# Kernel tuning notes

Hardware: AMD Instinct MI355X
Metric: run time of the kernel (lower is better)

The kernel has to match this reference:

```python
import jax, jax.numpy as jnp
import numpy as np

N, D = 2048, 1024
H, KV, HD = 16, 4, 64
REPEATS = H // KV
SCALE = HD ** -0.5


def setup_inputs() -> dict:
    key = jax.random.key(0)
    ks = jax.random.split(key, 6)
    x = jax.random.normal(ks[0], (N, D), dtype=jnp.float32)
    # rotary tables: cos/sin of interleaved-pair angles (llama-style view_as_complex)
    pos = jnp.arange(N, dtype=jnp.float32)[:, None]
    inv_freq = 1.0 / (10000.0 ** (jnp.arange(0, HD, 2, dtype=jnp.float32) / HD))
    ang = pos * inv_freq[None, :]  # (N, HD//2)
    freqs_cos = jnp.cos(ang)
    freqs_sin = jnp.sin(ang)
    s = 0.02
    Wq = jax.random.normal(ks[1], (D, H * HD), dtype=jnp.float32) * s
    Wk = jax.random.normal(ks[2], (D, KV * HD), dtype=jnp.float32) * s
    Wv = jax.random.normal(ks[3], (D, KV * HD), dtype=jnp.float32) * s
    Wo = jax.random.normal(ks[4], (H * HD, D), dtype=jnp.float32) * s
    return {"x": x, "freqs_cos": freqs_cos, "freqs_sin": freqs_sin,
            "Wq": Wq, "Wk": Wk, "Wv": Wv, "Wo": Wo}


def _rope(t, cos, sin):
    # t: (N, heads, HD); interleaved complex pairs (even=real, odd=imag)
    tr = t[..., 0::2]
    ti = t[..., 1::2]
    c = cos[:, None, :]
    s = sin[:, None, :]
    out_r = tr * c - ti * s
    out_i = tr * s + ti * c
    return jnp.stack([out_r, out_i], axis=-1).reshape(t.shape)


def reference(x, freqs_cos, freqs_sin, Wq, Wk, Wv, Wo):
    n = x.shape[0]
    xq = (x @ Wq).reshape(n, H, HD)
    xk = (x @ Wk).reshape(n, KV, HD)
    xv = (x @ Wv).reshape(n, KV, HD)
    xq = _rope(xq, freqs_cos, freqs_sin)
    xk = _rope(xk, freqs_cos, freqs_sin)
    # repeat_kv along head dim (GQA)
    k = jnp.repeat(xk, REPEATS, axis=1)  # (n, H, HD)
    v = jnp.repeat(xv, REPEATS, axis=1)
    # memory_efficient_attention with mask=None: full attention over token axis
    scores = jnp.einsum('nhd,mhd->hnm', xq, k) * SCALE
    attn = jax.nn.softmax(scores, axis=-1)
    out = jnp.einsum('hnm,mhd->nhd', attn, v)
    return out.reshape(n, H * HD) @ Wo
```

## Files before the change

kernel.cpp:

```cpp
#include <hip/hip_runtime.h>

#define N_TOK 2048
#define DMODEL 1024
#define NH 16
#define NKV 4
#define HDIM 64
#define SCALE_LOG2E 0.1803368801111204f

typedef __attribute__((ext_vector_type(8))) short short8;
typedef __attribute__((ext_vector_type(4))) float f32x4;
typedef unsigned short u16;
typedef unsigned int u32;

__device__ __forceinline__ u16 f2bf(float x) {
    u32 u = __float_as_uint(x);
    u += 0x7FFF + ((u >> 16) & 1);
    return (u16)(u >> 16);
}
__device__ __forceinline__ u32 pack2(float a, float b) {
    return (u32)f2bf(a) | ((u32)f2bf(b) << 16);
}
__device__ __forceinline__ u32 pack2t(float a, float b) {
    return __builtin_amdgcn_perm(__float_as_uint(b), __float_as_uint(a), 0x07060302u);
}

__global__ __launch_bounds__(256) void prep(
    const float* __restrict__ Wq, const float* __restrict__ Wk,
    const float* __restrict__ Wv, const float* __restrict__ Wo,
    const float* __restrict__ x,
    u16* __restrict__ Wqt, u16* __restrict__ Wkt, u16* __restrict__ Wvt,
    u16* __restrict__ Wot, u16* __restrict__ xb)
{
    const int z = blockIdx.z;
    const int t = threadIdx.x;
    if (z == 4) {
        size_t base = ((size_t)(blockIdx.y * 16 + blockIdx.x)) * 8192;
#pragma unroll
        for (int i = 0; i < 8; ++i) {
            float4 v = *(const float4*)(x + base + i * 1024 + t * 4);
            uint2 p; p.x = pack2(v.x, v.y); p.y = pack2(v.z, v.w);
            *(uint2*)(xb + base + i * 1024 + t * 4) = p;
        }
        return;
    }
    const float* W; u16* Wt; int NC;
    if      (z == 0) { W = Wq; Wt = Wqt; NC = 1024; }
    else if (z == 1) { W = Wk; Wt = Wkt; NC = 256; }
    else if (z == 2) { W = Wv; Wt = Wvt; NC = 256; }
    else             { W = Wo; Wt = Wot; NC = 1024; }
    const int n0 = blockIdx.x * 64;
    if (n0 >= NC) return;
    const int k0 = blockIdx.y * 64;
    __shared__ float T[64][68];
    const int row = t >> 2, cs = (t & 3) * 16;
#pragma unroll
    for (int i = 0; i < 4; ++i)
        *(float4*)&T[row][cs + i * 4] =
            *(const float4*)(W + (size_t)(k0 + row) * NC + n0 + cs + i * 4);
    __syncthreads();
    const int nl = t >> 2, ks = (t & 3) * 16;
    u32 pk[8];
#pragma unroll
    for (int i = 0; i < 8; ++i)
        pk[i] = pack2(T[ks + 2 * i][nl], T[ks + 2 * i + 1][nl]);
    u16* dst = Wt + (size_t)(n0 + nl) * DMODEL + k0 + ks;
    uint4 w0; w0.x = pk[0]; w0.y = pk[1]; w0.z = pk[2]; w0.w = pk[3];
    uint4 w1; w1.x = pk[4]; w1.y = pk[5]; w1.z = pk[6]; w1.w = pk[7];
    *(uint4*)(dst) = w0;
    *(uint4*)(dst + 8) = w1;
}

__global__ __launch_bounds__(256, 2) void gemm_qkv(
    const u16* __restrict__ A,
    const u16* __restrict__ B0, const u16* __restrict__ B1, const u16* __restrict__ B2,
    u16* __restrict__ D0, u16* __restrict__ D1, u16* __restrict__ FVout,
    const float* __restrict__ fc, const float* __restrict__ fs)
{
    __shared__ u16 As[128][40];
    __shared__ u16 Bs[128][40];
    const int t = threadIdx.x;
    const int m0 = blockIdx.x * 128;
    const int by = blockIdx.y;

    const u16* Bt; int nl0, ep;
    u16* dbf = nullptr; int dstride = 0; float epsc = 1.f;
    if (by < 8)       { Bt = B0; nl0 = by * 128;        dbf = D0; ep = 1; dstride = 1024;
                        epsc = SCALE_LOG2E; }
    else if (by < 10) { Bt = B1; nl0 = (by - 8) * 128;  dbf = D1; ep = 1; dstride = 256; }
    else              { Bt = B2; nl0 = (by - 10) * 128; ep = 2; }

    const int w = t >> 6, lane = t & 63;
    const int quad = lane >> 4, l15 = lane & 15;
    const int wm = (w >> 1) * 64, wn = (w & 1) * 64;
    const int srow = t >> 1, sk = (t & 1) * 16;

    const u16* Ap = A + (size_t)(m0 + srow) * DMODEL + sk;
    const u16* Bp = Bt + (size_t)(nl0 + srow) * DMODEL + sk;

    f32x4 acc[4][4];
#pragma unroll
    for (int i = 0; i < 4; ++i)
#pragma unroll
        for (int j = 0; j < 4; ++j) acc[i][j] = {0.f, 0.f, 0.f, 0.f};

    uint4 ar0 = *(const uint4*)(Ap);
    uint4 ar1 = *(const uint4*)(Ap + 8);
    uint4 br0 = *(const uint4*)(Bp);
    uint4 br1 = *(const uint4*)(Bp + 8);

    for (int k0 = 0; k0 < DMODEL; k0 += 32) {
        __syncthreads();
        *(uint4*)&As[srow][sk]     = ar0;
        *(uint4*)&As[srow][sk + 8] = ar1;
        *(uint4*)&Bs[srow][sk]     = br0;
        *(uint4*)&Bs[srow][sk + 8] = br1;
        __syncthreads();
        if (k0 + 32 < DMODEL) {
            ar0 = *(const uint4*)(Ap + k0 + 32);
            ar1 = *(const uint4*)(Ap + k0 + 40);
            br0 = *(const uint4*)(Bp + k0 + 32);
            br1 = *(const uint4*)(Bp + k0 + 40);
        }
        short8 af[4], bf[4];
#pragma unroll
        for (int i = 0; i < 4; ++i)
            af[i] = *(const short8*)&As[wm + i * 16 + l15][quad * 8];
#pragma unroll
        for (int j = 0; j < 4; ++j)
            bf[j] = *(const short8*)&Bs[wn + j * 16 + l15][quad * 8];
#pragma unroll
        for (int i = 0; i < 4; ++i)
#pragma unroll
            for (int j = 0; j < 4; ++j)
                acc[i][j] = __builtin_amdgcn_mfma_f32_16x16x32_bf16(af[i], bf[j], acc[i][j], 0, 0, 0);
    }

#pragma unroll
    for (int i = 0; i < 4; ++i)
#pragma unroll
        for (int j = 0; j < 4; ++j) {
            const int cl = nl0 + wn + j * 16 + l15;
#pragma unroll
            for (int r4 = 0; r4 < 4; ++r4) {
                const int r = m0 + wm + i * 16 + quad * 4 + r4;
                float own = acc[i][j][r4];
                if (ep == 1) {
                    float other = __shfl_xor(own, 1, 64);
                    const int p = (cl & 63) >> 1;
                    const float c = fc[r * 32 + p] * epsc, s = fs[r * 32 + p] * epsc;
                    float outv = ((cl & 1) == 0) ? (own * c - other * s)
                                                 : (other * s + own * c);
                    dbf[(size_t)r * dstride + cl] = f2bf(outv);
                } else {
                    const int g = cl >> 6, d = cl & 63;
                    const int dt = d >> 4, l15v = d & 15;
                    const int kt = r >> 6, klo = r & 63;
                    const int c = klo >> 5, k5 = klo & 31;
                    const int qd = k5 >> 3, jv = k5 & 7;
                    size_t idx = ((((size_t)(g * 32 + kt) * 4 + dt) * 2 + c) * 64
                                  + qd * 16 + l15v) * 8 + jv;
                    FVout[idx] = f2bf(own);
                }
            }
        }
}

__global__ __launch_bounds__(256, 2) void gemm_out(
    const u16* __restrict__ A, const u16* __restrict__ Bt, float* __restrict__ Dout)
{
    __shared__ u16 As[64][40];
    __shared__ u16 Bs[128][40];
    const int t = threadIdx.x;
    const int m0 = blockIdx.x * 64;
    const int nl0 = blockIdx.y * 128;

    const int w = t >> 6, lane = t & 63;
    const int quad = lane >> 4, l15 = lane & 15;
    const int wm = (w >> 1) * 32, wn = (w & 1) * 64;
    const int arow = t >> 2, acol = (t & 3) * 8;
    const int brow = t >> 1, bcol = (t & 1) * 16;

    const u16* Ap = A + (size_t)(m0 + arow) * DMODEL + acol;
    const u16* Bp = Bt + (size_t)(nl0 + brow) * DMODEL + bcol;

    f32x4 acc[2][4];
#pragma unroll
    for (int i = 0; i < 2; ++i)
#pragma unroll
        for (int j = 0; j < 4; ++j) acc[i][j] = {0.f, 0.f, 0.f, 0.f};

    uint4 ar  = *(const uint4*)(Ap);
    uint4 br0 = *(const uint4*)(Bp);
    uint4 br1 = *(const uint4*)(Bp + 8);

    for (int k0 = 0; k0 < DMODEL; k0 += 32) {
        __syncthreads();
        *(uint4*)&As[arow][acol]     = ar;
        *(uint4*)&Bs[brow][bcol]     = br0;
        *(uint4*)&Bs[brow][bcol + 8] = br1;
        __syncthreads();
        if (k0 + 32 < DMODEL) {
            ar  = *(const uint4*)(Ap + k0 + 32);
            br0 = *(const uint4*)(Bp + k0 + 32);
            br1 = *(const uint4*)(Bp + k0 + 40);
        }
        short8 af[2], bf[4];
#pragma unroll
        for (int i = 0; i < 2; ++i)
            af[i] = *(const short8*)&As[wm + i * 16 + l15][quad * 8];
#pragma unroll
        for (int j = 0; j < 4; ++j)
            bf[j] = *(const short8*)&Bs[wn + j * 16 + l15][quad * 8];
#pragma unroll
        for (int i = 0; i < 2; ++i)
#pragma unroll
            for (int j = 0; j < 4; ++j)
                acc[i][j] = __builtin_amdgcn_mfma_f32_16x16x32_bf16(af[i], bf[j], acc[i][j], 0, 0, 0);
    }

#pragma unroll
    for (int i = 0; i < 2; ++i)
#pragma unroll
        for (int j = 0; j < 4; ++j) {
            const int cl = nl0 + wn + j * 16 + l15;
#pragma unroll
            for (int r4 = 0; r4 < 4; ++r4) {
                const int r = m0 + wm + i * 16 + quad * 4 + r4;
                Dout[(size_t)r * 1024 + cl] = acc[i][j][r4];
            }
        }
}

__global__ __launch_bounds__(256, 2) void attn(
    const u16* __restrict__ Qb, const u16* __restrict__ Kb,
    const u16* __restrict__ FV, u16* __restrict__ Ob)
{
    __shared__ u16 Ks[2][128][72];
    __shared__ u16 Ps[4][2][16][68];

    const int t = threadIdx.x;
    const int n0 = blockIdx.x * 64;
    const int h = blockIdx.y, kvh = h >> 2;
    const int w = t >> 6, lane = t & 63;
    const int quad = lane >> 4, l15 = lane & 15;
    const int srow = t >> 1, ssel = (t & 1) * 32;

    const u16* qp = Qb + (size_t)(n0 + w * 16 + l15) * (NH * HDIM) + h * HDIM + quad * 8;
    const short8 aq0 = *(const short8*)qp;
    const short8 aq1 = *(const short8*)(qp + 32);

    const u16* kbase = Kb + (size_t)srow * (NKV * HDIM) + kvh * HDIM + ssel;
    const u16* fvb = FV + ((size_t)kvh * 32 * 4096) + (size_t)lane * 8;

    f32x4 o[4];
#pragma unroll
    for (int i = 0; i < 4; ++i) o[i] = {0.f, 0.f, 0.f, 0.f};
    float l_acc = 0.f;

#pragma unroll
    for (int c = 0; c < 4; ++c)
        *(uint4*)&Ks[0][srow][ssel + c * 8] = *(const uint4*)(kbase + c * 8);
    __syncthreads();

    for (int rd = 0; rd < 16; ++rd) {
        const int cur = rd & 1, nxt = cur ^ 1;
        const int rdn = (rd + 1) & 15;
        uint4 kr[4];
#pragma unroll
        for (int c = 0; c < 4; ++c)
            kr[c] = *(const uint4*)(kbase + (size_t)(rdn * 128) * (NKV * HDIM) + c * 8);

#pragma unroll
        for (int sub = 0; sub < 2; ++sub) {
            const int kt = rd * 2 + sub;
            short8 vf0[4], vf1[4];
#pragma unroll
            for (int dt = 0; dt < 4; ++dt) {
                vf0[dt] = *(const short8*)(fvb + (size_t)kt * 4096 + (dt * 2 + 0) * 512);
                vf1[dt] = *(const short8*)(fvb + (size_t)kt * 4096 + (dt * 2 + 1) * 512);
            }
            f32x4 s[4];
#pragma unroll
            for (int nt = 0; nt < 4; ++nt) {
                short8 kb0 = *(const short8*)&Ks[cur][sub * 64 + nt * 16 + l15][quad * 8];
                short8 kb1 = *(const short8*)&Ks[cur][sub * 64 + nt * 16 + l15][quad * 8 + 32];
                f32x4 z = {0.f, 0.f, 0.f, 0.f};
                z = __builtin_amdgcn_mfma_f32_16x16x32_bf16(kb0, aq0, z, 0, 0, 0);
                z = __builtin_amdgcn_mfma_f32_16x16x32_bf16(kb1, aq1, z, 0, 0, 0);
                s[nt] = z;
            }
#pragma unroll
            for (int nt = 0; nt < 4; ++nt) {
                float p0 = __builtin_amdgcn_exp2f(s[nt][0]);
                float p1 = __builtin_amdgcn_exp2f(s[nt][1]);
                float p2 = __builtin_amdgcn_exp2f(s[nt][2]);
                float p3 = __builtin_amdgcn_exp2f(s[nt][3]);
                l_acc += (p0 + p1) + (p2 + p3);
                uint2 pk; pk.x = pack2t(p0, p1); pk.y = pack2t(p2, p3);
                *(uint2*)&Ps[w][sub][l15][nt * 16 + quad * 4] = pk;
            }
            const short8 ap0 = *(const short8*)&Ps[w][sub][l15][quad * 8];
            const short8 ap1 = *(const short8*)&Ps[w][sub][l15][quad * 8 + 32];
#pragma unroll
            for (int dt = 0; dt < 4; ++dt) {
                o[dt] = __builtin_amdgcn_mfma_f32_16x16x32_bf16(ap0, vf0[dt], o[dt], 0, 0, 0);
                o[dt] = __builtin_amdgcn_mfma_f32_16x16x32_bf16(ap1, vf1[dt], o[dt], 0, 0, 0);
            }
        }
#pragma unroll
        for (int c = 0; c < 4; ++c)
            *(uint4*)&Ks[nxt][srow][ssel + c * 8] = kr[c];
        __syncthreads();
    }

    l_acc += __shfl_xor(l_acc, 16, 64);
    l_acc += __shfl_xor(l_acc, 32, 64);
    float linv[4];
#pragma unroll
    for (int r = 0; r < 4; ++r)
        linv[r] = 1.f / __shfl(l_acc, quad * 4 + r, 16);
#pragma unroll
    for (int dt = 0; dt < 4; ++dt)
#pragma unroll
        for (int r = 0; r < 4; ++r) {
            const int qrow = n0 + w * 16 + quad * 4 + r;
            const int col = h * HDIM + dt * 16 + l15;
            Ob[(size_t)qrow * (NH * HDIM) + col] = f2bf(o[dt][r] * linv[r]);
        }
}

extern "C" void kernel_launch(void* const* d_in, const int* in_sizes, int n_in,
                              void* d_out, int out_size, void* d_ws, size_t ws_size,
                              hipStream_t stream) {
    const float* x  = (const float*)d_in[0];
    const float* fc = (const float*)d_in[1];
    const float* fs = (const float*)d_in[2];
    const float* Wq = (const float*)d_in[3];
    const float* Wk = (const float*)d_in[4];
    const float* Wv = (const float*)d_in[5];
    const float* Wo = (const float*)d_in[6];
    float* out = (float*)d_out;

    u16* ws  = (u16*)d_ws;
    u16* xb  = ws;
    u16* Wqt = xb  + (size_t)2048 * 1024;
    u16* Wkt = Wqt + (size_t)1024 * 1024;
    u16* Wvt = Wkt + (size_t)256 * 1024;
    u16* Wot = Wvt + (size_t)256 * 1024;
    u16* qb  = Wot + (size_t)1024 * 1024;
    u16* kb  = qb  + (size_t)2048 * 1024;
    u16* fv  = kb  + (size_t)2048 * 256;
    u16* aob = fv  + (size_t)256 * 2048;

    prep<<<dim3(16, 16, 5), dim3(256), 0, stream>>>(Wq, Wk, Wv, Wo, x,
                                                    Wqt, Wkt, Wvt, Wot, xb);
    gemm_qkv<<<dim3(16, 12), dim3(256), 0, stream>>>(xb, Wqt, Wkt, Wvt,
                                                     qb, kb, fv, fc, fs);
    attn<<<dim3(32, 16), dim3(256), 0, stream>>>(qb, kb, fv, aob);
    gemm_out<<<dim3(32, 8), dim3(256), 0, stream>>>(aob, Wot, out);
}
```

Measured before the change: 157.6 us.

## Fuse all four stages into one cooperative persistent kernel with grid syncs

Replaces the four separate launches (prep, QKV GEMM, attention, output GEMM) with one cooperative kernel of 512 blocks that reuses a shared-memory union and separates the stages with grid-wide syncs. The QKV GEMM tile also shrinks from 128x128 to 64x128, so 384 blocks run instead of 192. This removes launch gaps and inter-kernel drains. In exchange it adds grid-sync overhead, leaves blocks idle in the GEMM stages, and sizes every block's shared memory to the largest stage, which may limit occupancy.

```diff
diff --git a/kernel.cpp b/kernel.cpp
--- a/kernel.cpp
+++ b/kernel.cpp
@@ -1,4 +1,7 @@
 #include <hip/hip_runtime.h>
+#include <hip/hip_cooperative_groups.h>
+
+namespace cg = cooperative_groups;
 
 #define N_TOK 2048
 #define DMODEL 1024
@@ -24,309 +27,305 @@
     return __builtin_amdgcn_perm(__float_as_uint(b), __float_as_uint(a), 0x07060302u);
 }
 
-__global__ __launch_bounds__(256) void prep(
+struct SmemPrep { float T[64][68]; };
+struct SmemGemm { u16 As[128][40]; u16 Bs[128][40]; };
+struct SmemAttn { u16 Ks[2][128][72]; u16 Ps[4][2][16][68]; };
+
+__global__ __launch_bounds__(256, 2) void fused(
+    const float* __restrict__ x, const float* __restrict__ fc,
+    const float* __restrict__ fs,
     const float* __restrict__ Wq, const float* __restrict__ Wk,
     const float* __restrict__ Wv, const float* __restrict__ Wo,
-    const float* __restrict__ x,
     u16* __restrict__ Wqt, u16* __restrict__ Wkt, u16* __restrict__ Wvt,
-    u16* __restrict__ Wot, u16* __restrict__ xb)
+    u16* __restrict__ Wot, u16* __restrict__ xb,
+    u16* __restrict__ qb, u16* __restrict__ kb, u16* __restrict__ fv,
+    u16* __restrict__ aob, float* __restrict__ out)
 {
-    const int z = blockIdx.z;
+    __shared__ alignas(16) char smem[sizeof(SmemAttn)];
     const int t = threadIdx.x;
-    if (z == 4) {
-        size_t base = ((size_t)(blockIdx.y * 16 + blockIdx.x)) * 8192;
-#pragma unroll
-        for (int i = 0; i < 8; ++i) {
-            float4 v = *(const float4*)(x + base + i * 1024 + t * 4);
-            uint2 p; p.x = pack2(v.x, v.y); p.y = pack2(v.z, v.w);
-            *(uint2*)(xb + base + i * 1024 + t * 4) = p;
+    const int bid = blockIdx.x;
+    cg::grid_group grid = cg::this_grid();
+
+    {
+        float (&T)[64][68] = reinterpret_cast<SmemPrep*>(smem)->T;
+        for (int j = bid; j < 896; j += 512) {
+            if (j >= 640) {
+                size_t base = (size_t)(j - 640) * 8192;
+#pragma unroll
+                for (int i = 0; i < 8; ++i) {
+                    float4 v = *(const float4*)(x + base + i * 1024 + t * 4);
+                    uint2 p; p.x = pack2(v.x, v.y); p.y = pack2(v.z, v.w);
+                    *(uint2*)(xb + base + i * 1024 + t * 4) = p;
+                }
+                continue;
+            }
+            const float* W; u16* Wt; int NC, xb_, yb_;
+            if (j < 256)      { W = Wq; Wt = Wqt; NC = 1024; xb_ = j & 15; yb_ = j >> 4; }
+            else if (j < 320) { W = Wk; Wt = Wkt; NC = 256;  int q = j - 256; xb_ = q & 3; yb_ = q >> 2; }
+            else if (j < 384) { W = Wv; Wt = Wvt; NC = 256;  int q = j - 320; xb_ = q & 3; yb_ = q >> 2; }
+            else              { W = Wo; Wt = Wot; NC = 1024; int q = j - 384; xb_ = q & 15; yb_ = q >> 4; }
+            const int n0 = xb_ * 64, k0 = yb_ * 64;
+            const int row = t >> 2, cs = (t & 3) * 16;
+            __syncthreads();
+#pragma unroll
+            for (int i = 0; i < 4; ++i)
+                *(float4*)&T[row][cs + i * 4] =
+                    *(const float4*)(W + (size_t)(k0 + row) * NC + n0 + cs + i * 4);
+            __syncthreads();
+            const int nl = t >> 2, ks = (t & 3) * 16;
+            u32 pk[8];
+#pragma unroll
+            for (int i = 0; i < 8; ++i)
+                pk[i] = pack2(T[ks + 2 * i][nl], T[ks + 2 * i + 1][nl]);
+            u16* dst = Wt + (size_t)(n0 + nl) * DMODEL + k0 + ks;
+            uint4 w0; w0.x = pk[0]; w0.y = pk[1]; w0.z = pk[2]; w0.w = pk[3];
+            uint4 w1; w1.x = pk[4]; w1.y = pk[5]; w1.z = pk[6]; w1.w = pk[7];
+            *(uint4*)(dst) = w0;
+            *(uint4*)(dst + 8) = w1;
         }
-        return;
     }
-    const float* W; u16* Wt; int NC;
-    if      (z == 0) { W = Wq; Wt = Wqt; NC = 1024; }
-    else if (z == 1) { W = Wk; Wt = Wkt; NC = 256; }
-    else if (z == 2) { W = Wv; Wt = Wvt; NC = 256; }
-    else             { W = Wo; Wt = Wot; NC = 1024; }
-    const int n0 = blockIdx.x * 64;
-    if (n0 >= NC) return;
-    const int k0 = blockIdx.y * 64;
-    __shared__ float T[64][68];
-    const int row = t >> 2, cs = (t & 3) * 16;
-#pragma unroll
-    for (int i = 0; i < 4; ++i)
-        *(float4*)&T[row][cs + i * 4] =
-            *(const float4*)(W + (size_t)(k0 + row) * NC + n0 + cs + i * 4);
-    __syncthreads();
-    const int nl = t >> 2, ks = (t & 3) * 16;
-    u32 pk[8];
-#pragma unroll
-    for (int i = 0; i < 8; ++i)
-        pk[i] = pack2(T[ks + 2 * i][nl], T[ks + 2 * i + 1][nl]);
-    u16* dst = Wt + (size_t)(n0 + nl) * DMODEL + k0 + ks;
-    uint4 w0; w0.x = pk[0]; w0.y = pk[1]; w0.z = pk[2]; w0.w = pk[3];
-    uint4 w1; w1.x = pk[4]; w1.y = pk[5]; w1.z = pk[6]; w1.w = pk[7];
-    *(uint4*)(dst) = w0;
-    *(uint4*)(dst + 8) = w1;
-}
-
-__global__ __launch_bounds__(256, 2) void gemm_qkv(
-    const u16* __restrict__ A,
-    const u16* __restrict__ B0, const u16* __restrict__ B1, const u16* __restrict__ B2,
-    u16* __restrict__ D0, u16* __restrict__ D1, u16* __restrict__ FVout,
-    const float* __restrict__ fc, const float* __restrict__ fs)
-{
-    __shared__ u16 As[128][40];
-    __shared__ u16 Bs[128][40];
-    const int t = threadIdx.x;
-    const int m0 = blockIdx.x * 128;
-    const int by = blockIdx.y;
-
-    const u16* Bt; int nl0, ep;
-    u16* dbf = nullptr; int dstride = 0; float epsc = 1.f;
-    if (by < 8)       { Bt = B0; nl0 = by * 128;        dbf = D0; ep = 1; dstride = 1024;
-                        epsc = SCALE_LOG2E; }
-    else if (by < 10) { Bt = B1; nl0 = (by - 8) * 128;  dbf = D1; ep = 1; dstride = 256; }
-    else              { Bt = B2; nl0 = (by - 10) * 128; ep = 2; }
-
-    const int w = t >> 6, lane = t & 63;
-    const int quad = lane >> 4, l15 = lane & 15;
-    const int wm = (w >> 1) * 64, wn = (w & 1) * 64;
-    const int srow = t >> 1, sk = (t & 1) * 16;
-
-    const u16* Ap = A + (size_t)(m0 + srow) * DMODEL + sk;
-    const u16* Bp = Bt + (size_t)(nl0 + srow) * DMODEL + sk;
-
-    f32x4 acc[4][4];
-#pragma unroll
-    for (int i = 0; i < 4; ++i)
-#pragma unroll
-        for (int j = 0; j < 4; ++j) acc[i][j] = {0.f, 0.f, 0.f, 0.f};
-
-    uint4 ar0 = *(const uint4*)(Ap);
-    uint4 ar1 = *(const uint4*)(Ap + 8);
-    uint4 br0 = *(const uint4*)(Bp);
-    uint4 br1 = *(const uint4*)(Bp + 8);
-
-    for (int k0 = 0; k0 < DMODEL; k0 += 32) {
+    grid.sync();
+
+    if (bid < 384) {
+        SmemGemm* SG = reinterpret_cast<SmemGemm*>(smem);
+        const int m0 = (bid & 31) * 64;
+        const int by = bid >> 5;
+        const u16* Bt; int nl0, ep;
+        u16* dbf = nullptr; int dstride = 0; float epsc = 1.f;
+        if (by < 8)       { Bt = Wqt; nl0 = by * 128;        dbf = qb; ep = 1; dstride = 1024;
+                            epsc = SCALE_LOG2E; }
+        else if (by < 10) { Bt = Wkt; nl0 = (by - 8) * 128;  dbf = kb; ep = 1; dstride = 256; }
+        else              { Bt = Wvt; nl0 = (by - 10) * 128; ep = 2; }
+
+        const int w = t >> 6, lane = t & 63;
+        const int quad = lane >> 4, l15 = lane & 15;
+        const int wm = (w >> 1) * 32, wn = (w & 1) * 64;
+        const int arow = t >> 2, acol = (t & 3) * 8;
+        const int brow = t >> 1, bcol = (t & 1) * 16;
+
+        const u16* Ap = xb + (size_t)(m0 + arow) * DMODEL + acol;
+        const u16* Bp = Bt + (size_t)(nl0 + brow) * DMODEL + bcol;
+
+        f32x4 acc[2][4];
+#pragma unroll
+        for (int i = 0; i < 2; ++i)
+#pragma unroll
+            for (int j = 0; j < 4; ++j) acc[i][j] = {0.f, 0.f, 0.f, 0.f};
+
+        uint4 ar  = *(const uint4*)(Ap);
+        uint4 br0 = *(const uint4*)(Bp);
+        uint4 br1 = *(const uint4*)(Bp + 8);
+
+        for (int k0 = 0; k0 < DMODEL; k0 += 32) {
+            __syncthreads();
+            *(uint4*)&SG->As[arow][acol]     = ar;
+            *(uint4*)&SG->Bs[brow][bcol]     = br0;
+            *(uint4*)&SG->Bs[brow][bcol + 8] = br1;
+            __syncthreads();
+            if (k0 + 32 < DMODEL) {
+                ar  = *(const uint4*)(Ap + k0 + 32);
+                br0 = *(const uint4*)(Bp + k0 + 32);
+                br1 = *(const uint4*)(Bp + k0 + 40);
+            }
+            short8 af[2], bf[4];
+#pragma unroll
+            for (int i = 0; i < 2; ++i)
+                af[i] = *(const short8*)&SG->As[wm + i * 16 + l15][quad * 8];
+#pragma unroll
+            for (int j = 0; j < 4; ++j)
+                bf[j] = *(const short8*)&SG->Bs[wn + j * 16 + l15][quad * 8];
+#pragma unroll
+            for (int i = 0; i < 2; ++i)
+#pragma unroll
+                for (int j = 0; j < 4; ++j)
+                    acc[i][j] = __builtin_amdgcn_mfma_f32_16x16x32_bf16(af[i], bf[j], acc[i][j], 0, 0, 0);
+        }
+
+#pragma unroll
+        for (int i = 0; i < 2; ++i)
+#pragma unroll
+            for (int j = 0; j < 4; ++j) {
+                const int cl = nl0 + wn + j * 16 + l15;
+#pragma unroll
+                for (int r4 = 0; r4 < 4; ++r4) {
+                    const int r = m0 + wm + i * 16 + quad * 4 + r4;
+                    float own = acc[i][j][r4];
+                    if (ep == 1) {
+                        float other = __shfl_xor(own, 1, 64);
+                        const int p = (cl & 63) >> 1;
+                        const float c = fc[r * 32 + p] * epsc, s = fs[r * 32 + p] * epsc;
+                        float outv = ((cl & 1) == 0) ? (own * c - other * s)
+                                                     : (other * s + own * c);
+                        dbf[(size_t)r * dstride + cl] = f2bf(outv);
+                    } else {
+                        const int g = cl >> 6, d = cl & 63;
+                        const int dt = d >> 4, l15v = d & 15;
+                        const int kt = r >> 6, klo = r & 63;
+                        const int c = klo >> 5, k5 = klo & 31;
+                        const int qd = k5 >> 3, jv = k5 & 7;
+                        size_t idx = ((((size_t)(g * 32 + kt) * 4 + dt) * 2 + c) * 64
+                                      + qd * 16 + l15v) * 8 + jv;
+                        fv[idx] = f2bf(own);
+                    }
+                }
+            }
+    }
+    grid.sync();
+
+    {
+        SmemAttn* SA = reinterpret_cast<SmemAttn*>(smem);
+        const int n0 = (bid >> 4) * 64;
+        const int h = bid & 15, kvh = h >> 2;
+        const int w = t >> 6, lane = t & 63;
+        const int quad = lane >> 4, l15 = lane & 15;
+        const int srow = t >> 1, ssel = (t & 1) * 32;
+
+        const u16* qp = qb + (size_t)(n0 + w * 16 + l15) * (NH * HDIM) + h * HDIM + quad * 8;
+        const short8 aq0 = *(const short8*)qp;
+        const short8 aq1 = *(const short8*)(qp + 32);
+
+        const u16* kbase = kb + (size_t)srow * (NKV * HDIM) + kvh * HDIM + ssel;
+        const u16* fvb = fv + ((size_t)kvh * 32 * 4096) + (size_t)lane * 8;
+
+        f32x4 o[4];
+#pragma unroll
+        for (int i = 0; i < 4; ++i) o[i] = {0.f, 0.f, 0.f, 0.f};
+        float l_acc = 0.f;
+
+#pragma unroll
+        for (int c = 0; c < 4; ++c)
+            *(uint4*)&SA->Ks[0][srow][ssel + c * 8] = *(const uint4*)(kbase + c * 8);
         __syncthreads();
-        *(uint4*)&As[srow][sk]     = ar0;
-        *(uint4*)&As[srow][sk + 8] = ar1;
-        *(uint4*)&Bs[srow][sk]     = br0;
-        *(uint4*)&Bs[srow][sk + 8] = br1;
-        __syncthreads();
-        if (k0 + 32 < DMODEL) {
-            ar0 = *(const uint4*)(Ap + k0 + 32);
-            ar1 = *(const uint4*)(Ap + k0 + 40);
-            br0 = *(const uint4*)(Bp + k0 + 32);
-            br1 = *(const uint4*)(Bp + k0 + 40);
+
+        for (int rd = 0; rd < 16; ++rd) {
+            const int cur = rd & 1, nxt = cur ^ 1;
+            const int rdn = (rd + 1) & 15;
+            uint4 kr[4];
+#pragma unroll
+            for (int c = 0; c < 4; ++c)
+                kr[c] = *(const uint4*)(kbase + (size_t)(rdn * 128) * (NKV * HDIM) + c * 8);
+
+#pragma unroll
+            for (int sub = 0; sub < 2; ++sub) {
+                const int kt = rd * 2 + sub;
+                short8 vf0[4], vf1[4];
+#pragma unroll
+                for (int dt = 0; dt < 4; ++dt) {
+                    vf0[dt] = *(const short8*)(fvb + (size_t)kt * 4096 + (dt * 2 + 0) * 512);
+                    vf1[dt] = *(const short8*)(fvb + (size_t)kt * 4096 + (dt * 2 + 1) * 512);
+                }
+                f32x4 s[4];
+#pragma unroll
+                for (int nt = 0; nt < 4; ++nt) {
+                    short8 kb0 = *(const short8*)&SA->Ks[cur][sub * 64 + nt * 16 + l15][quad * 8];
+                    short8 kb1 = *(const short8*)&SA->Ks[cur][sub * 64 + nt * 16 + l15][quad * 8 + 32];
+                    f32x4 z = {0.f, 0.f, 0.f, 0.f};
+                    z = __builtin_amdgcn_mfma_f32_16x16x32_bf16(kb0, aq0, z, 0, 0, 0);
+                    z = __builtin_amdgcn_mfma_f32_16x16x32_bf16(kb1, aq1, z, 0, 0, 0);
+                    s[nt] = z;
+                }
+#pragma unroll
+                for (int nt = 0; nt < 4; ++nt) {
+                    float p0 = __builtin_amdgcn_exp2f(s[nt][0]);
+                    float p1 = __builtin_amdgcn_exp2f(s[nt][1]);
+                    float p2 = __builtin_amdgcn_exp2f(s[nt][2]);
+                    float p3 = __builtin_amdgcn_exp2f(s[nt][3]);
+                    l_acc += (p0 + p1) + (p2 + p3);
+                    uint2 pk; pk.x = pack2t(p0, p1); pk.y = pack2t(p2, p3);
+                    *(uint2*)&SA->Ps[w][sub][l15][nt * 16 + quad * 4] = pk;
+                }
+                const short8 ap0 = *(const short8*)&SA->Ps[w][sub][l15][quad * 8];
+                const short8 ap1 = *(const short8*)&SA->Ps[w][sub][l15][quad * 8 + 32];
+#pragma unroll
+                for (int dt = 0; dt < 4; ++dt) {
+                    o[dt] = __builtin_amdgcn_mfma_f32_16x16x32_bf16(ap0, vf0[dt], o[dt], 0, 0, 0);
+                    o[dt] = __builtin_amdgcn_mfma_f32_16x16x32_bf16(ap1, vf1[dt], o[dt], 0, 0, 0);
+                }
+            }
+#pragma unroll
+            for (int c = 0; c < 4; ++c)
+                *(uint4*)&SA->Ks[nxt][srow][ssel + c * 8] = kr[c];
+            __syncthreads();
         }
-        short8 af[4], bf[4];
-#pragma unroll
-        for (int i = 0; i < 4; ++i)
-            af[i] = *(const short8*)&As[wm + i * 16 + l15][quad * 8];
-#pragma unroll
-        for (int j = 0; j < 4; ++j)
-            bf[j] = *(const short8*)&Bs[wn + j * 16 + l15][quad * 8];
-#pragma unroll
-        for (int i = 0; i < 4; ++i)
+
+        l_acc += __shfl_xor(l_acc, 16, 64);
+        l_acc += __shfl_xor(l_acc, 32, 64);
+        float linv[4];
+#pragma unroll
+        for (int r = 0; r < 4; ++r)
+            linv[r] = 1.f / __shfl(l_acc, quad * 4 + r, 16);
+#pragma unroll
+        for (int dt = 0; dt < 4; ++dt)
+#pragma unroll
+            for (int r = 0; r < 4; ++r) {
+                const int qrow = n0 + w * 16 + quad * 4 + r;
+                const int col = h * HDIM + dt * 16 + l15;
+                aob[(size_t)qrow * (NH * HDIM) + col] = f2bf(o[dt][r] * linv[r]);
+            }
+    }
+    grid.sync();
+
+    if (bid < 256) {
+        SmemGemm* SG = reinterpret_cast<SmemGemm*>(smem);
+        const int m0 = (bid & 31) * 64;
+        const int nl0 = (bid >> 5) * 128;
+
+        const int w = t >> 6, lane = t & 63;
+        const int quad = lane >> 4, l15 = lane & 15;
+        const int wm = (w >> 1) * 32, wn = (w & 1) * 64;
+        const int arow = t >> 2, acol = (t & 3) * 8;
+        const int brow = t >> 1, bcol = (t & 1) * 16;
+
+        const u16* Ap = aob + (size_t)(m0 + arow) * DMODEL + acol;
+        const u16* Bp = Wot + (size_t)(nl0 + brow) * DMODEL + bcol;
+
+        f32x4 acc[2][4];
+#pragma unroll
+        for (int i = 0; i < 2; ++i)
+#pragma unroll
+            for (int j = 0; j < 4; ++j) acc[i][j] = {0.f, 0.f, 0.f, 0.f};
+
+        uint4 ar  = *(const uint4*)(Ap);
+        uint4 br0 = *(const uint4*)(Bp);
+        uint4 br1 = *(const uint4*)(Bp + 8);
+
+        for (int k0 = 0; k0 < DMODEL; k0 += 32) {
+            __syncthreads();
+            *(uint4*)&SG->As[arow][acol]     = ar;
+            *(uint4*)&SG->Bs[brow][bcol]     = br0;
+            *(uint4*)&SG->Bs[brow][bcol + 8] = br1;
+            __syncthreads();
+            if (k0 + 32 < DMODEL) {
+                ar  = *(const uint4*)(Ap + k0 + 32);
+                br0 = *(const uint4*)(Bp + k0 + 32);
+                br1 = *(const uint4*)(Bp + k0 + 40);
+            }
+            short8 af[2], bf[4];
+#pragma unroll
+            for (int i = 0; i < 2; ++i)
+                af[i] = *(const short8*)&SG->As[wm + i * 16 + l15][quad * 8];
 #pragma unroll
             for (int j = 0; j < 4; ++j)
-                acc[i][j] = __builtin_amdgcn_mfma_f32_16x16x32_bf16(af[i], bf[j], acc[i][j], 0, 0, 0);
+                bf[j] = *(const short8*)&SG->Bs[wn + j * 16 + l15][quad * 8];
+#pragma unroll
+            for (int i = 0; i < 2; ++i)
+#pragma unroll
+                for (int j = 0; j < 4; ++j)
+                    acc[i][j] = __builtin_amdgcn_mfma_f32_16x16x32_bf16(af[i], bf[j], acc[i][j], 0, 0, 0);
+        }
+
+#pragma unroll
+        for (int i = 0; i < 2; ++i)
+#pragma unroll
+            for (int j = 0; j < 4; ++j) {
+                const int cl = nl0 + wn + j * 16 + l15;
+#pragma unroll
+                for (int r4 = 0; r4 < 4; ++r4) {
+                    const int r = m0 + wm + i * 16 + quad * 4 + r4;
+                    out[(size_t)r * 1024 + cl] = acc[i][j][r4];
+                }
+            }
     }
-
-#pragma unroll
-    for (int i = 0; i < 4; ++i)
-#pragma unroll
-        for (int j = 0; j < 4; ++j) {
-            const int cl = nl0 + wn + j * 16 + l15;
-#pragma unroll
-            for (int r4 = 0; r4 < 4; ++r4) {
-                const int r = m0 + wm + i * 16 + quad * 4 + r4;
-                float own = acc[i][j][r4];
-                if (ep == 1) {
-                    float other = __shfl_xor(own, 1, 64);
-                    const int p = (cl & 63) >> 1;
-                    const float c = fc[r * 32 + p] * epsc, s = fs[r * 32 + p] * epsc;
-                    float outv = ((cl & 1) == 0) ? (own * c - other * s)
-                                                 : (other * s + own * c);
-                    dbf[(size_t)r * dstride + cl] = f2bf(outv);
-                } else {
-                    const int g = cl >> 6, d = cl & 63;
-                    const int dt = d >> 4, l15v = d & 15;
-                    const int kt = r >> 6, klo = r & 63;
-                    const int c = klo >> 5, k5 = klo & 31;
-                    const int qd = k5 >> 3, jv = k5 & 7;
-                    size_t idx = ((((size_t)(g * 32 + kt) * 4 + dt) * 2 + c) * 64
-                                  + qd * 16 + l15v) * 8 + jv;
-                    FVout[idx] = f2bf(own);
-                }
-            }
-        }
-}
-
-__global__ __launch_bounds__(256, 2) void gemm_out(
-    const u16* __restrict__ A, const u16* __restrict__ Bt, float* __restrict__ Dout)
-{
-    __shared__ u16 As[64][40];
-    __shared__ u16 Bs[128][40];
-    const int t = threadIdx.x;
-    const int m0 = blockIdx.x * 64;
-    const int nl0 = blockIdx.y * 128;
-
-    const int w = t >> 6, lane = t & 63;
-    const int quad = lane >> 4, l15 = lane & 15;
-    const int wm = (w >> 1) * 32, wn = (w & 1) * 64;
-    const int arow = t >> 2, acol = (t & 3) * 8;
-    const int brow = t >> 1, bcol = (t & 1) * 16;
-
-    const u16* Ap = A + (size_t)(m0 + arow) * DMODEL + acol;
-    const u16* Bp = Bt + (size_t)(nl0 + brow) * DMODEL + bcol;
-
-    f32x4 acc[2][4];
-#pragma unroll
-    for (int i = 0; i < 2; ++i)
-#pragma unroll
-        for (int j = 0; j < 4; ++j) acc[i][j] = {0.f, 0.f, 0.f, 0.f};
-
-    uint4 ar  = *(const uint4*)(Ap);
-    uint4 br0 = *(const uint4*)(Bp);
-    uint4 br1 = *(const uint4*)(Bp + 8);
-
-    for (int k0 = 0; k0 < DMODEL; k0 += 32) {
-        __syncthreads();
-        *(uint4*)&As[arow][acol]     = ar;
-        *(uint4*)&Bs[brow][bcol]     = br0;
-        *(uint4*)&Bs[brow][bcol + 8] = br1;
-        __syncthreads();
-        if (k0 + 32 < DMODEL) {
-            ar  = *(const uint4*)(Ap + k0 + 32);
-            br0 = *(const uint4*)(Bp + k0 + 32);
-            br1 = *(const uint4*)(Bp + k0 + 40);
-        }
-        short8 af[2], bf[4];
-#pragma unroll
-        for (int i = 0; i < 2; ++i)
-            af[i] = *(const short8*)&As[wm + i * 16 + l15][quad * 8];
-#pragma unroll
-        for (int j = 0; j < 4; ++j)
-            bf[j] = *(const short8*)&Bs[wn + j * 16 + l15][quad * 8];
-#pragma unroll
-        for (int i = 0; i < 2; ++i)
-#pragma unroll
-            for (int j = 0; j < 4; ++j)
-                acc[i][j] = __builtin_amdgcn_mfma_f32_16x16x32_bf16(af[i], bf[j], acc[i][j], 0, 0, 0);
-    }
-
-#pragma unroll
-    for (int i = 0; i < 2; ++i)
-#pragma unroll
-        for (int j = 0; j < 4; ++j) {
-            const int cl = nl0 + wn + j * 16 + l15;
-#pragma unroll
-            for (int r4 = 0; r4 < 4; ++r4) {
-                const int r = m0 + wm + i * 16 + quad * 4 + r4;
-                Dout[(size_t)r * 1024 + cl] = acc[i][j][r4];
-            }
-        }
-}
-
-__global__ __launch_bounds__(256, 2) void attn(
-    const u16* __restrict__ Qb, const u16* __restrict__ Kb,
-    const u16* __restrict__ FV, u16* __restrict__ Ob)
-{
-    __shared__ u16 Ks[2][128][72];
-    __shared__ u16 Ps[4][2][16][68];
-
-    const int t = threadIdx.x;
-    const int n0 = blockIdx.x * 64;
-    const int h = blockIdx.y, kvh = h >> 2;
-    const int w = t >> 6, lane = t & 63;
-    const int quad = lane >> 4, l15 = lane & 15;
-    const int srow = t >> 1, ssel = (t & 1) * 32;
-
-    const u16* qp = Qb + (size_t)(n0 + w * 16 + l15) * (NH * HDIM) + h * HDIM + quad * 8;
-    const short8 aq0 = *(const short8*)qp;
-    const short8 aq1 = *(const short8*)(qp + 32);
-
-    const u16* kbase = Kb + (size_t)srow * (NKV * HDIM) + kvh * HDIM + ssel;
-    const u16* fvb = FV + ((size_t)kvh * 32 * 4096) + (size_t)lane * 8;
-
-    f32x4 o[4];
-#pragma unroll
-    for (int i = 0; i < 4; ++i) o[i] = {0.f, 0.f, 0.f, 0.f};
-    float l_acc = 0.f;
-
-#pragma unroll
-    for (int c = 0; c < 4; ++c)
-        *(uint4*)&Ks[0][srow][ssel + c * 8] = *(const uint4*)(kbase + c * 8);
-    __syncthreads();
-
-    for (int rd = 0; rd < 16; ++rd) {
-        const int cur = rd & 1, nxt = cur ^ 1;
-        const int rdn = (rd + 1) & 15;
-        uint4 kr[4];
-#pragma unroll
-        for (int c = 0; c < 4; ++c)
-            kr[c] = *(const uint4*)(kbase + (size_t)(rdn * 128) * (NKV * HDIM) + c * 8);
-
-#pragma unroll
-        for (int sub = 0; sub < 2; ++sub) {
-            const int kt = rd * 2 + sub;
-            short8 vf0[4], vf1[4];
-#pragma unroll
-            for (int dt = 0; dt < 4; ++dt) {
-                vf0[dt] = *(const short8*)(fvb + (size_t)kt * 4096 + (dt * 2 + 0) * 512);
-                vf1[dt] = *(const short8*)(fvb + (size_t)kt * 4096 + (dt * 2 + 1) * 512);
-            }
-            f32x4 s[4];
-#pragma unroll
-            for (int nt = 0; nt < 4; ++nt) {
-                short8 kb0 = *(const short8*)&Ks[cur][sub * 64 + nt * 16 + l15][quad * 8];
-                short8 kb1 = *(const short8*)&Ks[cur][sub * 64 + nt * 16 + l15][quad * 8 + 32];
-                f32x4 z = {0.f, 0.f, 0.f, 0.f};
-                z = __builtin_amdgcn_mfma_f32_16x16x32_bf16(kb0, aq0, z, 0, 0, 0);
-                z = __builtin_amdgcn_mfma_f32_16x16x32_bf16(kb1, aq1, z, 0, 0, 0);
-                s[nt] = z;
-            }
-#pragma unroll
-            for (int nt = 0; nt < 4; ++nt) {
-                float p0 = __builtin_amdgcn_exp2f(s[nt][0]);
-                float p1 = __builtin_amdgcn_exp2f(s[nt][1]);
-                float p2 = __builtin_amdgcn_exp2f(s[nt][2]);
-                float p3 = __builtin_amdgcn_exp2f(s[nt][3]);
-                l_acc += (p0 + p1) + (p2 + p3);
-                uint2 pk; pk.x = pack2t(p0, p1); pk.y = pack2t(p2, p3);
-                *(uint2*)&Ps[w][sub][l15][nt * 16 + quad * 4] = pk;
-            }
-            const short8 ap0 = *(const short8*)&Ps[w][sub][l15][quad * 8];
-            const short8 ap1 = *(const short8*)&Ps[w][sub][l15][quad * 8 + 32];
-#pragma unroll
-            for (int dt = 0; dt < 4; ++dt) {
-                o[dt] = __builtin_amdgcn_mfma_f32_16x16x32_bf16(ap0, vf0[dt], o[dt], 0, 0, 0);
-                o[dt] = __builtin_amdgcn_mfma_f32_16x16x32_bf16(ap1, vf1[dt], o[dt], 0, 0, 0);
-            }
-        }
-#pragma unroll
-        for (int c = 0; c < 4; ++c)
-            *(uint4*)&Ks[nxt][srow][ssel + c * 8] = kr[c];
-        __syncthreads();
-    }
-
-    l_acc += __shfl_xor(l_acc, 16, 64);
-    l_acc += __shfl_xor(l_acc, 32, 64);
-    float linv[4];
-#pragma unroll
-    for (int r = 0; r < 4; ++r)
-        linv[r] = 1.f / __shfl(l_acc, quad * 4 + r, 16);
-#pragma unroll
-    for (int dt = 0; dt < 4; ++dt)
-#pragma unroll
-        for (int r = 0; r < 4; ++r) {
-            const int qrow = n0 + w * 16 + quad * 4 + r;
-            const int col = h * HDIM + dt * 16 + l15;
-            Ob[(size_t)qrow * (NH * HDIM) + col] = f2bf(o[dt][r] * linv[r]);
-        }
 }
 
 extern "C" void kernel_launch(void* const* d_in, const int* in_sizes, int n_in,
@@ -352,10 +351,12 @@
     u16* fv  = kb  + (size_t)2048 * 256;
     u16* aob = fv  + (size_t)256 * 2048;
 
-    prep<<<dim3(16, 16, 5), dim3(256), 0, stream>>>(Wq, Wk, Wv, Wo, x,
-                                                    Wqt, Wkt, Wvt, Wot, xb);
-    gemm_qkv<<<dim3(16, 12), dim3(256), 0, stream>>>(xb, Wqt, Wkt, Wvt,
-                                                     qb, kb, fv, fc, fs);
-    attn<<<dim3(32, 16), dim3(256), 0, stream>>>(qb, kb, fv, aob);
-    gemm_out<<<dim3(32, 8), dim3(256), 0, stream>>>(aob, Wot, out);
-}
+    void* args[] = {
+        (void*)&x, (void*)&fc, (void*)&fs,
+        (void*)&Wq, (void*)&Wk, (void*)&Wv, (void*)&Wo,
+        (void*)&Wqt, (void*)&Wkt, (void*)&Wvt, (void*)&Wot, (void*)&xb,
+        (void*)&qb, (void*)&kb, (void*)&fv, (void*)&aob, (void*)&out
+    };
+    hipLaunchCooperativeKernel((const void*)fused, dim3(512), dim3(256),
+                               args, 0, stream);
+}
```

After: 358.1 us. 127% more time.
